# Kernel optimization log

Hardware: AMD Instinct MI355X
Metric: run time of the kernel (lower is better)

## Reference

```python
import jax, jax.numpy as jnp
import numpy as np

N_NODES = 100000
N_EDGES = 1600000
IN_F = 128
OUT_F = 64
LN_EPS = 1e-5


def setup_inputs() -> dict:
    key = jax.random.key(0)
    ks = jax.random.split(key, 8)
    stdv = 1.0 / np.sqrt(OUT_F)
    x = jax.random.normal(ks[0], (N_NODES, IN_F), dtype=jnp.float32)
    weight = jax.random.uniform(ks[1], (IN_F, OUT_F), minval=-stdv, maxval=stdv, dtype=jnp.float32)
    bias = jnp.zeros((OUT_F,), dtype=jnp.float32)
    ln_gamma = jnp.ones((OUT_F,), dtype=jnp.float32)
    ln_beta = jnp.zeros((OUT_F,), dtype=jnp.float32)
    # residual nn.Linear(in_features, out_features): weight [out, in], bias [out]
    bound = 1.0 / np.sqrt(IN_F)
    res_w = jax.random.uniform(ks[2], (OUT_F, IN_F), minval=-bound, maxval=bound, dtype=jnp.float32)
    res_b = jax.random.uniform(ks[3], (OUT_F,), minval=-bound, maxval=bound, dtype=jnp.float32)
    edge_src = jax.random.randint(ks[4], (N_EDGES,), 0, N_NODES, dtype=jnp.int64 if jax.config.jax_enable_x64 else jnp.int32)
    edge_dst = jax.random.randint(ks[5], (N_EDGES,), 0, N_NODES, dtype=jnp.int64 if jax.config.jax_enable_x64 else jnp.int32)
    edge_weight = jax.random.uniform(ks[6], (N_EDGES,), dtype=jnp.float32)
    return {
        "x": x, "weight": weight, "bias": bias,
        "ln_gamma": ln_gamma, "ln_beta": ln_beta,
        "res_w": res_w, "res_b": res_b,
        "edge_weight": edge_weight, "edge_src": edge_src, "edge_dst": edge_dst,
    }


def reference(x, weight, bias, ln_gamma, ln_beta, res_w, res_b, edge_weight, edge_src, edge_dst):
    # support = x @ W                                   [N, OUT_F]
    support = x @ weight
    # spmm: out[d] = sum_{e: dst(e)=d} w_e * support[src(e)]
    msg = support[edge_src] * edge_weight[:, None]      # [E, OUT_F]
    out = jax.ops.segment_sum(msg, edge_dst, num_segments=x.shape[0])
    # bias
    out = out + bias
    # layernorm over feature dim
    mu = jnp.mean(out, axis=-1, keepdims=True)
    var = jnp.var(out, axis=-1, keepdims=True)
    out = (out - mu) * jax.lax.rsqrt(var + LN_EPS) * ln_gamma + ln_beta
    # relu activation
    out = jax.nn.relu(out)
    # residual linear on the input
    out = out + x @ res_w.T + res_b
    return out
```

## Files before the change

kernel.cpp:

```cpp
#include <hip/hip_runtime.h>

#define N_NODES 100000
#define N_EDGES 1600000
#define IN_F 128
#define OUT_F 64
#define LN_EPS 1e-5f

#define BSHIFT 6
#define BNODES 64
#define NB ((N_NODES + BNODES - 1) >> BSHIFT)

#define CAP 2048
#define CH 2048

#define MT 64
#define NGEMM ((N_NODES + MT - 1) / MT)
#define LDA 136

#define K1_BLOCKS 768
#define K1_GEMM_BLOCKS 512
#define K1_PART_BLOCKS 256
#define K1_THREADS 256
#define K1_PART_CHUNK ((N_EDGES + K1_PART_BLOCKS - 1) / K1_PART_BLOCKS)

typedef __attribute__((ext_vector_type(8))) short short8;
typedef __attribute__((ext_vector_type(4))) short short4v;
typedef __attribute__((ext_vector_type(4))) float f32x4;

__device__ __forceinline__ unsigned short f2bf(float f) {
  unsigned int u = __float_as_uint(f);
  unsigned int r = (u + 0x7FFFu + ((u >> 16) & 1u)) >> 16;
  return (unsigned short)r;
}
__device__ __forceinline__ float bf2f(unsigned short h) {
  return __uint_as_float((unsigned int)h << 16);
}

__global__ __launch_bounds__(K1_THREADS) void gemm_partition(
    const float* __restrict__ x, const float* __restrict__ W,
    const float* __restrict__ res_w, const float* __restrict__ res_b,
    const int* __restrict__ esrc, const int* __restrict__ edst,
    const float* __restrict__ ew, unsigned short* __restrict__ support,
    float* __restrict__ resid, int* __restrict__ gcount,
    int2* __restrict__ part) {
  __shared__ __align__(16) char smem[52224];
  const int tid = threadIdx.x;
  const int bid = blockIdx.x;

  if (bid < K1_GEMM_BLOCKS) {
    short* bt = (short*)smem;
    short* al = (short*)(smem + 34816);

    for (int i = tid; i < 128 * 64; i += K1_THREADS) {
      const int k = i >> 6, n = i & 63;
      bt[n * LDA + k] = (short)f2bf(W[i]);
    }
    for (int i = tid; i < 64 * 128; i += K1_THREADS) {
      const int np = i >> 7, k = i & 127;
      bt[(64 + np) * LDA + k] = (short)f2bf(res_w[i]);
    }

    const int w = tid >> 6;
    const int lane = tid & 63;
    const int m16 = lane & 15;
    const int quad = lane >> 4;

    float rbv[8];
#pragma unroll
    for (int nt = 0; nt < 8; ++nt)
      rbv[nt] = (nt >= 4) ? res_b[nt * 16 + m16 - 64] : 0.f;

    for (int g = bid; g < NGEMM; g += K1_GEMM_BLOCKS) {
      __syncthreads();

      const size_t row0 = (size_t)g * MT;
      for (int i = tid; i < MT * 32; i += K1_THREADS) {
        const int r = i >> 5, c4 = i & 31;
        const size_t grow = row0 + r;
        float4 v = make_float4(0.f, 0.f, 0.f, 0.f);
        if (grow < N_NODES) v = ((const float4*)x)[grow * 32 + c4];
        short4v p;
        p.x = (short)f2bf(v.x); p.y = (short)f2bf(v.y);
        p.z = (short)f2bf(v.z); p.w = (short)f2bf(v.w);
        *(short4v*)(&al[r * LDA + c4 * 4]) = p;
      }
      __syncthreads();

      short8 afr[4];
#pragma unroll
      for (int kt = 0; kt < 4; ++kt)
        afr[kt] = *(const short8*)(&al[(w * 16 + m16) * LDA + kt * 32 + quad * 8]);

#pragma unroll
      for (int nt = 0; nt < 8; ++nt) {
        f32x4 acc = {0.f, 0.f, 0.f, 0.f};
#pragma unroll
        for (int kt = 0; kt < 4; ++kt) {
          const short8 bfr =
              *(const short8*)(&bt[(nt * 16 + m16) * LDA + kt * 32 + quad * 8]);
          acc = __builtin_amdgcn_mfma_f32_16x16x32_bf16(afr[kt], bfr, acc, 0, 0, 0);
        }
        const int col = nt * 16 + m16;
#pragma unroll
        for (int r = 0; r < 4; ++r) {
          const size_t row = row0 + w * 16 + quad * 4 + r;
          if (row < N_NODES) {
            if (col < 64) support[row * OUT_F + col] = f2bf(acc[r]);
            else          resid[row * OUT_F + (col - 64)] = acc[r] + rbv[nt];
          }
        }
      }
    }
  } else {
    int* lcnt = (int*)smem;
    int* lpos = (int*)(smem + 6256);
    for (int i = tid; i < NB; i += K1_THREADS) lcnt[i] = 0;
    __syncthreads();
    const int pb = bid - K1_GEMM_BLOCKS;
    const int beg = pb * K1_PART_CHUNK;
    const int end = min(beg + K1_PART_CHUNK, N_EDGES);
    for (int i = beg + tid; i < end; i += K1_THREADS)
      atomicAdd(&lcnt[edst[i] >> BSHIFT], 1);
    __syncthreads();
    for (int i = tid; i < NB; i += K1_THREADS)
      lpos[i] = lcnt[i] ? atomicAdd(&gcount[i], lcnt[i]) : 0;
    __syncthreads();
    for (int i = beg + tid; i < end; i += K1_THREADS) {
      const int d = edst[i];
      const int b = d >> BSHIFT;
      const int p = atomicAdd(&lpos[b], 1);
      part[(size_t)b * CAP + p] =
          make_int2((esrc[i] << BSHIFT) | (d & 63), __float_as_int(ew[i]));
    }
  }
}

__global__ __launch_bounds__(512, 4) void bucket_sort_accum(
    const unsigned short* __restrict__ support, const int2* __restrict__ part,
    const int* __restrict__ gcount, const float* __restrict__ resid,
    const float* __restrict__ bias, const float* __restrict__ gamma,
    const float* __restrict__ beta, float* __restrict__ out) {
  __shared__ int2 estage[CH];
  __shared__ int2 esorted[CH];
  __shared__ int bcnt2[BNODES];
  __shared__ int bseg[BNODES];
  __shared__ int bpos[BNODES];
  const int tid = threadIdx.x;
  const int o = tid & 63;
  const int wid = tid >> 6;
  const int b = blockIdx.x;
  const int cnt = min(gcount[b], CAP);
  const size_t beg = (size_t)b * CAP;
  const size_t end = beg + cnt;

  float acc8[8];
#pragma unroll
  for (int t = 0; t < 8; ++t) acc8[t] = 0.f;

  for (size_t base = beg; base < end; base += CH) {
    const int n = (int)min((size_t)CH, end - base);
    __syncthreads();
    if (tid < BNODES) bcnt2[tid] = 0;
    __syncthreads();

    for (int i = tid; i < n; i += 512) {
      const int2 r = part[base + i];
      estage[i] = r;
      atomicAdd(&bcnt2[r.x & 63], 1);
    }
    __syncthreads();

    if (wid == 0) {
      const int v = bcnt2[o];
      int incl = v;
#pragma unroll
      for (int off = 1; off < 64; off <<= 1) {
        const int u = __shfl_up(incl, off, 64);
        if (o >= off) incl += u;
      }
      bseg[o] = incl - v;
      bpos[o] = incl - v;
    }
    __syncthreads();

    for (int i = tid; i < n; i += 512) {
      const int2 r = estage[i];
      const int p = atomicAdd(&bpos[r.x & 63], 1);
      esorted[p] = r;
    }
    __syncthreads();

#pragma unroll
    for (int t = 0; t < 8; ++t) {
      const int j = wid * 8 + t;
      const int s = bseg[j];
      const int c = bcnt2[j];
      float a = acc8[t];
      int e = 0;
      for (; e + 4 <= c; e += 4) {
        const int2 m0 = esorted[s + e + 0];
        const int2 m1 = esorted[s + e + 1];
        const int2 m2 = esorted[s + e + 2];
        const int2 m3 = esorted[s + e + 3];
        const float v0 = bf2f(support[((size_t)((unsigned)m0.x >> 6) << 6) + o]);
        const float v1 = bf2f(support[((size_t)((unsigned)m1.x >> 6) << 6) + o]);
        const float v2 = bf2f(support[((size_t)((unsigned)m2.x >> 6) << 6) + o]);
        const float v3 = bf2f(support[((size_t)((unsigned)m3.x >> 6) << 6) + o]);
        a = fmaf(v0, __int_as_float(m0.y), a);
        a = fmaf(v1, __int_as_float(m1.y), a);
        a = fmaf(v2, __int_as_float(m2.y), a);
        a = fmaf(v3, __int_as_float(m3.y), a);
      }
      for (; e < c; ++e) {
        const int2 m = esorted[s + e];
        a = fmaf(bf2f(support[((size_t)((unsigned)m.x >> 6) << 6) + o]),
                 __int_as_float(m.y), a);
      }
      acc8[t] = a;
    }
  }

  const float bi = bias[o];
  const float ga = gamma[o];
  const float be = beta[o];
#pragma unroll
  for (int t = 0; t < 8; ++t) {
    const int j = wid * 8 + t;
    const int nid = (b << BSHIFT) + j;
    if (nid < N_NODES) {
      const float v = acc8[t] + bi;
      float s = v, sq = v * v;
#pragma unroll
      for (int off = 32; off > 0; off >>= 1) {
        s += __shfl_xor(s, off, 64);
        sq += __shfl_xor(sq, off, 64);
      }
      const float mu = s * (1.f / 64.f);
      const float var = sq * (1.f / 64.f) - mu * mu;
      const float r = rsqrtf(var + LN_EPS);
      const float nrm = fmaxf((v - mu) * r * ga + be, 0.f);
      out[(size_t)nid * OUT_F + o] = nrm + resid[(size_t)nid * OUT_F + o];
    }
  }
}

extern "C" void kernel_launch(void* const* d_in, const int* in_sizes, int n_in,
                              void* d_out, int out_size, void* d_ws,
                              size_t ws_size, hipStream_t stream) {
  const float* x      = (const float*)d_in[0];
  const float* weight = (const float*)d_in[1];
  const float* bias   = (const float*)d_in[2];
  const float* gamma  = (const float*)d_in[3];
  const float* beta   = (const float*)d_in[4];
  const float* res_w  = (const float*)d_in[5];
  const float* res_b  = (const float*)d_in[6];
  const float* ew     = (const float*)d_in[7];
  const int*   esrc   = (const int*)d_in[8];
  const int*   edst   = (const int*)d_in[9];
  float* out = (float*)d_out;

  char* ws = (char*)d_ws;
  size_t off = 0;
  auto alloc = [&](size_t bytes) {
    void* p = ws + off;
    off += (bytes + 255) & ~(size_t)255;
    return p;
  };
  unsigned short* support = (unsigned short*)alloc((size_t)N_NODES * OUT_F * 2);
  float* resid   = (float*)alloc((size_t)N_NODES * OUT_F * sizeof(float));
  int2*  part    = (int2*)alloc((size_t)NB * CAP * sizeof(int2));
  int*   gcount  = (int*)alloc((size_t)NB * sizeof(int));

  hipMemsetAsync(gcount, 0, (size_t)NB * sizeof(int), stream);

  gemm_partition<<<K1_BLOCKS, K1_THREADS, 0, stream>>>(
      x, weight, res_w, res_b, esrc, edst, ew, support, resid, gcount, part);
  bucket_sort_accum<<<NB, 512, 0, stream>>>(support, part, gcount, resid,
                                            bias, gamma, beta, out);
}
```

Baseline: 220.9 us.

## Load GEMM A fragments directly from global memory and rebalance block split

The GEMM blocks now read x rows straight from global memory into MFMA A-fragment registers and convert them to bf16 there, instead of staging them through shared memory. This removes the per-tile shared-memory store/load and two barriers, and shrinks shared memory so more blocks can be resident. The grid is also enlarged, giving the GEMM and the edge partition phase more blocks each. Global reads are now per-lane 32-byte strided loads that may coalesce less well than the previous cooperative loads.

```diff
diff --git a/kernel.cpp b/kernel.cpp
--- a/kernel.cpp
+++ b/kernel.cpp
@@ -17,14 +17,13 @@
 #define NGEMM ((N_NODES + MT - 1) / MT)
 #define LDA 136
 
-#define K1_BLOCKS 768
-#define K1_GEMM_BLOCKS 512
-#define K1_PART_BLOCKS 256
+#define K1_GEMM_BLOCKS 768
+#define K1_PART_BLOCKS 512
+#define K1_BLOCKS (K1_GEMM_BLOCKS + K1_PART_BLOCKS)
 #define K1_THREADS 256
 #define K1_PART_CHUNK ((N_EDGES + K1_PART_BLOCKS - 1) / K1_PART_BLOCKS)
 
 typedef __attribute__((ext_vector_type(8))) short short8;
-typedef __attribute__((ext_vector_type(4))) short short4v;
 typedef __attribute__((ext_vector_type(4))) float f32x4;
 
 __device__ __forceinline__ unsigned short f2bf(float f) {
@@ -43,13 +42,12 @@
     const float* __restrict__ ew, unsigned short* __restrict__ support,
     float* __restrict__ resid, int* __restrict__ gcount,
     int2* __restrict__ part) {
-  __shared__ __align__(16) char smem[52224];
+  __shared__ __align__(16) char smem[34816];
   const int tid = threadIdx.x;
   const int bid = blockIdx.x;
 
   if (bid < K1_GEMM_BLOCKS) {
     short* bt = (short*)smem;
-    short* al = (short*)(smem + 34816);
 
     for (int i = tid; i < 128 * 64; i += K1_THREADS) {
       const int k = i >> 6, n = i & 63;
@@ -59,6 +57,7 @@
       const int np = i >> 7, k = i & 127;
       bt[(64 + np) * LDA + k] = (short)f2bf(res_w[i]);
     }
+    __syncthreads();
 
     const int w = tid >> 6;
     const int lane = tid & 63;
@@ -70,26 +69,30 @@
     for (int nt = 0; nt < 8; ++nt)
       rbv[nt] = (nt >= 4) ? res_b[nt * 16 + m16 - 64] : 0.f;
 
+    const float4* xr = (const float4*)x;
+
     for (int g = bid; g < NGEMM; g += K1_GEMM_BLOCKS) {
-      __syncthreads();
-
       const size_t row0 = (size_t)g * MT;
-      for (int i = tid; i < MT * 32; i += K1_THREADS) {
-        const int r = i >> 5, c4 = i & 31;
-        const size_t grow = row0 + r;
+      const size_t arow = row0 + (size_t)(w * 16 + m16);
+      const bool ok = arow < N_NODES;
+      const size_t abase = arow * 32 + quad * 2;
+
+      short8 afr[4];
+#pragma unroll
+      for (int kt = 0; kt < 4; ++kt) {
+        float4 u = make_float4(0.f, 0.f, 0.f, 0.f);
         float4 v = make_float4(0.f, 0.f, 0.f, 0.f);
-        if (grow < N_NODES) v = ((const float4*)x)[grow * 32 + c4];
-        short4v p;
-        p.x = (short)f2bf(v.x); p.y = (short)f2bf(v.y);
-        p.z = (short)f2bf(v.z); p.w = (short)f2bf(v.w);
-        *(short4v*)(&al[r * LDA + c4 * 4]) = p;
-      }
-      __syncthreads();
-
-      short8 afr[4];
-#pragma unroll
-      for (int kt = 0; kt < 4; ++kt)
-        afr[kt] = *(const short8*)(&al[(w * 16 + m16) * LDA + kt * 32 + quad * 8]);
+        if (ok) {
+          u = xr[abase + kt * 8];
+          v = xr[abase + kt * 8 + 1];
+        }
+        short8 a;
+        a[0] = (short)f2bf(u.x); a[1] = (short)f2bf(u.y);
+        a[2] = (short)f2bf(u.z); a[3] = (short)f2bf(u.w);
+        a[4] = (short)f2bf(v.x); a[5] = (short)f2bf(v.y);
+        a[6] = (short)f2bf(v.z); a[7] = (short)f2bf(v.w);
+        afr[kt] = a;
+      }
 
 #pragma unroll
       for (int nt = 0; nt < 8; ++nt) {
```

Result: no change. 219.7 us (-0.5%).
